# Optimization experiments

Hardware: AMD Instinct MI355X
Metric: run time of the kernel (lower is better)

Reference implementation:

```python
import jax, jax.numpy as jnp
import numpy as np

N, E, D_IN, H, L, B, D_OUT = 50000, 800000, 128, 128, 3, 512, 64
BN_EPS = 1e-5


def _leaky(v):
    return jax.nn.leaky_relu(v, 0.2)


def _bn_eval(v, g, b):
    # eval-mode BatchNorm1d with running_mean=0, running_var=1
    return g * v * (1.0 / np.sqrt(1.0 + BN_EPS)) + b


def setup_inputs() -> dict:
    key = jax.random.key(0)
    ks = jax.random.split(key, 12)
    s = 0.02  # weight init scale
    return {
        "x": jax.random.normal(ks[0], (N, D_IN), jnp.float32),
        "edge_index": jax.random.randint(ks[1], (2, E), 0, N, jnp.int64),
        "batch": jnp.sort(jax.random.randint(ks[2], (N,), 0, B, jnp.int64)),
        "node_W": jax.random.normal(ks[3], (D_IN, H), jnp.float32) * s,
        "node_b": jnp.zeros((H,), jnp.float32),
        "conv_W1": jax.random.normal(ks[4], (L, H, H), jnp.float32) * s,
        "conv_b1": jnp.zeros((L, H), jnp.float32),
        "conv_g": jnp.ones((L, H), jnp.float32),
        "conv_beta": jnp.zeros((L, H), jnp.float32),
        "conv_W2": jax.random.normal(ks[5], (L, H, H), jnp.float32) * s,
        "conv_b2": jnp.zeros((L, H), jnp.float32),
        "vn_emb": jax.random.normal(ks[6], (1, H), jnp.float32) * s,
        "vn_W1": jax.random.normal(ks[7], (L, H, H), jnp.float32) * s,
        "vn_b1": jnp.zeros((L, H), jnp.float32),
        "vn_W2": jax.random.normal(ks[8], (L, H, H), jnp.float32) * s,
        "vn_b2": jnp.zeros((L, H), jnp.float32),
        "bn_g": jnp.ones((H,), jnp.float32),
        "bn_b": jnp.zeros((H,), jnp.float32),
        "fc_W": jax.random.normal(ks[9], (D_OUT, H), jnp.float32) * s,
        "fc_b": jnp.zeros((D_OUT,), jnp.float32),
    }


def reference(x, edge_index, batch, node_W, node_b, conv_W1, conv_b1, conv_g,
              conv_beta, conv_W2, conv_b2, vn_emb, vn_W1, vn_b1, vn_W2, vn_b2,
              bn_g, bn_b, fc_W, fc_b):
    src, dst = edge_index[0], edge_index[1]
    h = x @ node_W + node_b                              # [N, H]
    vn = jnp.broadcast_to(vn_emb, (B, vn_emb.shape[1]))  # [B, H]
    counts = jax.ops.segment_sum(jnp.ones((h.shape[0],), h.dtype), batch,
                                 num_segments=B)          # [B]
    denom = jnp.maximum(counts, 1.0)[:, None]
    for l in range(L):
        h = h + vn[batch]
        # GINConv (eps=0): mlp((1+eps)*x + sum of neighbor messages)
        agg = jax.ops.segment_sum(h[src], dst, num_segments=h.shape[0])
        z = h + agg
        z = _leaky(z @ conv_W1[l] + conv_b1[l])
        z = _bn_eval(z, conv_g[l], conv_beta[l])
        h = _leaky(z @ conv_W2[l] + conv_b2[l])
        # dropout is identity in eval mode
        vn_update = jax.ops.segment_sum(h, batch, num_segments=B) / denom
        vn = vn + (_leaky(vn_update @ vn_W1[l] + vn_b1[l]) @ vn_W2[l] + vn_b2[l])
    out = jax.ops.segment_sum(h, batch, num_segments=B)   # global_add_pool
    out = _bn_eval(out, bn_g, bn_b)
    return out @ fc_W.T + fc_b                            # [B, D_OUT]
```

## Files before the change

kernel.cpp:

```cpp
#include <hip/hip_runtime.h>
#include <hip/hip_bf16.h>

#define NN 50000
#define NE 800000
#define NB 512
#define WT_S 136
#define WT_M (128 * WT_S)
#define DCAP 64

using u32 = unsigned int;
using u16 = unsigned short;
typedef __attribute__((ext_vector_type(8))) short short8;
typedef __attribute__((ext_vector_type(4))) float f32x4;

constexpr float BNS = 0.9999950000374998f;

__device__ inline u16 f2bf(float f) {
    u32 b = __builtin_bit_cast(u32, f);
    return (u16)((b + 0x7FFFu + ((b >> 16) & 1u)) >> 16);
}
__device__ inline float bf2f(u32 u) {
    return __builtin_bit_cast(float, u << 16);
}
__device__ inline u32 pk2(float a, float b) {
    return (u32)f2bf(a) | ((u32)f2bf(b) << 16);
}

__global__ void k_wprep(const float* __restrict__ nW, const float* __restrict__ cW1,
                        const float* __restrict__ cW2, u16* __restrict__ wt) {
    int idx = blockIdx.x * 256 + threadIdx.x;
    int m = idx >> 14, e = idx & 16383;
    int k = e >> 7, c = e & 127;
    const float* src = m == 0 ? nW : (m <= 3 ? cW1 + (m - 1) * 16384 : cW2 + (m - 4) * 16384);
    wt[m * WT_M + c * WT_S + k] = f2bf(src[e]);
}

__global__ void k_setup(const float* __restrict__ vn_emb, float* __restrict__ vn,
                        u16* __restrict__ vnb, const int* __restrict__ batch,
                        int* __restrict__ bstart, float* __restrict__ counts) {
    int idx = blockIdx.x * 256 + threadIdx.x;
    if (idx < NB * 128) {
        float v = vn_emb[idx & 127];
        vn[idx] = v;
        vnb[idx] = f2bf(v);
    }
    if (idx <= NB) {
        int b = idx;
        int lo = 0, hi = NN;
        while (lo < hi) { int m = (lo + hi) >> 1; if (batch[m] < b) lo = m + 1; else hi = m; }
        bstart[b] = lo;
        if (b < NB) {
            int b1 = b + 1, lo1 = 0, hi1 = NN;
            while (lo1 < hi1) { int m = (lo1 + hi1) >> 1; if (batch[m] < b1) lo1 = m + 1; else hi1 = m; }
            counts[b] = (float)(lo1 - lo);
        }
    }
}

__global__ void k_pcsr(const int* __restrict__ ei, const int* __restrict__ batch,
                       int* __restrict__ deg, u32* __restrict__ nbr) {
    int e = blockIdx.x * 256 + threadIdx.x;
    if (e >= NE) return;
    int src = ei[e];
    int dst = ei[NE + e];
    int pos = atomicAdd(&deg[dst], 1);
    if (pos < DCAP) nbr[(size_t)dst * DCAP + pos] = (u32)src | ((u32)batch[src] << 16);
}

__global__ __launch_bounds__(256) void k_gather(
    const int* __restrict__ deg, const u32* __restrict__ nbr,
    const u16* __restrict__ hb0, const u16* __restrict__ vnb,
    const int* __restrict__ batch, u16* __restrict__ ah, u16* __restrict__ alo) {
    int node = blockIdx.x * 8 + (threadIdx.x >> 5);
    int q = threadIdx.x & 31;
    if (node >= NN) return;
    const uint2* h2 = (const uint2*)hb0;
    const uint2* v2 = (const uint2*)vnb;
    const u32* nb = nbr + (size_t)node * DCAP;
    int n = min(deg[node], DCAP);
    uint2 vd = h2[(size_t)node * 32 + q];
    uint2 wd = v2[(size_t)batch[node] * 32 + q];
    float4 A = {bf2f(vd.x & 0xFFFFu) + bf2f(wd.x & 0xFFFFu),
                bf2f(vd.x >> 16) + bf2f(wd.x >> 16),
                bf2f(vd.y & 0xFFFFu) + bf2f(wd.y & 0xFFFFu),
                bf2f(vd.y >> 16) + bf2f(wd.y >> 16)};
    float4 Bc = {0.f, 0.f, 0.f, 0.f};
    int j = 0;
    for (; j + 3 < n; j += 4) {
        uint4 nn = *(const uint4*)(nb + j);
        uint2 u0 = h2[(size_t)(nn.x & 0xFFFFu) * 32 + q];
        uint2 w0 = v2[(size_t)(nn.x >> 16) * 32 + q];
        uint2 u1 = h2[(size_t)(nn.y & 0xFFFFu) * 32 + q];
        uint2 w1 = v2[(size_t)(nn.y >> 16) * 32 + q];
        uint2 u2 = h2[(size_t)(nn.z & 0xFFFFu) * 32 + q];
        uint2 w2 = v2[(size_t)(nn.z >> 16) * 32 + q];
        uint2 u3 = h2[(size_t)(nn.w & 0xFFFFu) * 32 + q];
        uint2 w3 = v2[(size_t)(nn.w >> 16) * 32 + q];
        A.x += bf2f(u0.x & 0xFFFFu) + bf2f(w0.x & 0xFFFFu);
        A.y += bf2f(u0.x >> 16) + bf2f(w0.x >> 16);
        A.z += bf2f(u0.y & 0xFFFFu) + bf2f(w0.y & 0xFFFFu);
        A.w += bf2f(u0.y >> 16) + bf2f(w0.y >> 16);
        Bc.x += bf2f(u1.x & 0xFFFFu) + bf2f(w1.x & 0xFFFFu);
        Bc.y += bf2f(u1.x >> 16) + bf2f(w1.x >> 16);
        Bc.z += bf2f(u1.y & 0xFFFFu) + bf2f(w1.y & 0xFFFFu);
        Bc.w += bf2f(u1.y >> 16) + bf2f(w1.y >> 16);
        A.x += bf2f(u2.x & 0xFFFFu) + bf2f(w2.x & 0xFFFFu);
        A.y += bf2f(u2.x >> 16) + bf2f(w2.x >> 16);
        A.z += bf2f(u2.y & 0xFFFFu) + bf2f(w2.y & 0xFFFFu);
        A.w += bf2f(u2.y >> 16) + bf2f(w2.y >> 16);
        Bc.x += bf2f(u3.x & 0xFFFFu) + bf2f(w3.x & 0xFFFFu);
        Bc.y += bf2f(u3.x >> 16) + bf2f(w3.x >> 16);
        Bc.z += bf2f(u3.y & 0xFFFFu) + bf2f(w3.y & 0xFFFFu);
        Bc.w += bf2f(u3.y >> 16) + bf2f(w3.y >> 16);
    }
    for (; j < n; ++j) {
        u32 nn = nb[j];
        uint2 u0 = h2[(size_t)(nn & 0xFFFFu) * 32 + q];
        uint2 w0 = v2[(size_t)(nn >> 16) * 32 + q];
        A.x += bf2f(u0.x & 0xFFFFu) + bf2f(w0.x & 0xFFFFu);
        A.y += bf2f(u0.x >> 16) + bf2f(w0.x >> 16);
        A.z += bf2f(u0.y & 0xFFFFu) + bf2f(w0.y & 0xFFFFu);
        A.w += bf2f(u0.y >> 16) + bf2f(w0.y >> 16);
    }
    A.x += Bc.x; A.y += Bc.y; A.z += Bc.z; A.w += Bc.w;
    u16 h0 = f2bf(A.x), h1 = f2bf(A.y), h2_ = f2bf(A.z), h3 = f2bf(A.w);
    ((uint2*)ah)[(size_t)node * 32 + q] =
        make_uint2((u32)h0 | ((u32)h1 << 16), (u32)h2_ | ((u32)h3 << 16));
    ((uint2*)alo)[(size_t)node * 32 + q] =
        make_uint2(pk2(A.x - bf2f(h0), A.y - bf2f(h1)),
                   pk2(A.z - bf2f(h2_), A.w - bf2f(h3)));
}

template <int EPI, int AMODE, bool OBF16>
__global__ __launch_bounds__(512) void k_gemm(
    const void* __restrict__ Ap, const void* __restrict__ Ap2,
    const u16* __restrict__ wt, const float* __restrict__ bias,
    const float* __restrict__ gg, const float* __restrict__ bb,
    void* __restrict__ outp, int nrows) {
    __shared__ u16 sW[WT_M];
    const int t = threadIdx.x;
    {
        const float4* src = (const float4*)wt;
        float4* dst = (float4*)sW;
        for (int i = t; i < WT_M / 8; i += 512) dst[i] = src[i];
    }
    __syncthreads();
    const int lane = t & 63;
    const int w = t >> 6;
    const int rl = lane & 15;
    const int q = lane >> 4;
    const int rbase = blockIdx.x * 256 + w * 32;

    short8 af[2][4], al[2][4];
#pragma unroll
    for (int ri = 0; ri < 2; ++ri) {
        int row = min(rbase + ri * 16 + rl, nrows - 1);
#pragma unroll
        for (int kc = 0; kc < 4; ++kc) {
            if (AMODE == 2) {
                const float* ap = (const float*)Ap + (size_t)row * 128 + kc * 32 + q * 8;
                float4 f0 = *(const float4*)ap;
                float4 f1 = *(const float4*)(ap + 4);
                float fv[8] = {f0.x, f0.y, f0.z, f0.w, f1.x, f1.y, f1.z, f1.w};
                short8 hi, lo;
#pragma unroll
                for (int i = 0; i < 8; ++i) {
                    u16 hv = f2bf(fv[i]);
                    hi[i] = (short)hv;
                    lo[i] = (short)f2bf(fv[i] - bf2f(hv));
                }
                af[ri][kc] = hi;
                al[ri][kc] = lo;
            } else {
                af[ri][kc] = *(const short8*)((const u16*)Ap + (size_t)row * 128 + kc * 32 + q * 8);
                if (AMODE == 1)
                    al[ri][kc] = *(const short8*)((const u16*)Ap2 + (size_t)row * 128 + kc * 32 + q * 8);
            }
        }
    }

#pragma unroll
    for (int ct = 0; ct < 8; ++ct) {
        f32x4 acc0 = {0.f, 0.f, 0.f, 0.f};
        f32x4 acc1 = {0.f, 0.f, 0.f, 0.f};
#pragma unroll
        for (int kc = 0; kc < 4; ++kc) {
            short8 bf = *(const short8*)&sW[(ct * 16 + rl) * WT_S + kc * 32 + q * 8];
            if (AMODE != 0) {
                acc0 = __builtin_amdgcn_mfma_f32_16x16x32_bf16(al[0][kc], bf, acc0, 0, 0, 0);
                acc1 = __builtin_amdgcn_mfma_f32_16x16x32_bf16(al[1][kc], bf, acc1, 0, 0, 0);
            }
            acc0 = __builtin_amdgcn_mfma_f32_16x16x32_bf16(af[0][kc], bf, acc0, 0, 0, 0);
            acc1 = __builtin_amdgcn_mfma_f32_16x16x32_bf16(af[1][kc], bf, acc1, 0, 0, 0);
        }
        const int col = ct * 16 + rl;
        const float bs = bias[col];
        const float g = (EPI == 2) ? gg[col] : 0.f;
        const float be = (EPI == 2) ? bb[col] : 0.f;
#pragma unroll
        for (int half = 0; half < 2; ++half) {
            const f32x4& ac = half ? acc1 : acc0;
#pragma unroll
            for (int i = 0; i < 4; ++i) {
                int r = rbase + half * 16 + q * 4 + i;
                if (r < nrows) {
                    float v = ac[i] + bs;
                    if (EPI >= 1) v = v > 0.f ? v : 0.2f * v;
                    if (EPI == 2) v = g * v * BNS + be;
                    if (OBF16) ((u16*)outp)[(size_t)r * 128 + col] = f2bf(v);
                    else ((float*)outp)[(size_t)r * 128 + col] = v;
                }
            }
        }
    }
}

__global__ __launch_bounds__(256) void k_vnup(
    const u16* __restrict__ hb0, const int* __restrict__ bstart,
    const float* __restrict__ counts, const float* __restrict__ W1,
    const float* __restrict__ b1, const float* __restrict__ W2,
    const float* __restrict__ b2, float* __restrict__ vn, u16* __restrict__ vnb) {
    __shared__ float4 red[8][32];
    __shared__ float sP[128], sT[128], sH[2][128];
    const int b = blockIdx.x;
    const int t = threadIdx.x;
    const int s = bstart[b], e = bstart[b + 1];
    const int g = t >> 5, q = t & 31;
    const uint2* h2 = (const uint2*)hb0;
    float4 a = make_float4(0.f, 0.f, 0.f, 0.f);
    for (int r = s + g; r < e; r += 8) {
        uint2 v = h2[(size_t)r * 32 + q];
        a.x += bf2f(v.x & 0xFFFFu); a.y += bf2f(v.x >> 16);
        a.z += bf2f(v.y & 0xFFFFu); a.w += bf2f(v.y >> 16);
    }
    red[g][q] = a;
    __syncthreads();
    if (g == 0) {
#pragma unroll
        for (int g2 = 1; g2 < 8; ++g2) {
            float4 v = red[g2][q];
            a.x += v.x; a.y += v.y; a.z += v.z; a.w += v.w;
        }
        float inv = 1.f / fmaxf(counts[b], 1.f);
        sP[q * 4 + 0] = a.x * inv;
        sP[q * 4 + 1] = a.y * inv;
        sP[q * 4 + 2] = a.z * inv;
        sP[q * 4 + 3] = a.w * inv;
    }
    __syncthreads();
    {
        const int c = t & 127, hf = t >> 7;
        float acc = 0.f;
        const float* Wp = W1 + (size_t)(hf * 64) * 128 + c;
#pragma unroll 8
        for (int k = 0; k < 64; ++k) acc += sP[hf * 64 + k] * Wp[(size_t)k * 128];
        sH[hf][c] = acc;
    }
    __syncthreads();
    if (t < 128) {
        float v = sH[0][t] + sH[1][t] + b1[t];
        sT[t] = v > 0.f ? v : 0.2f * v;
    }
    __syncthreads();
    {
        const int c = t & 127, hf = t >> 7;
        float acc = 0.f;
        const float* Wp = W2 + (size_t)(hf * 64) * 128 + c;
#pragma unroll 8
        for (int k = 0; k < 64; ++k) acc += sT[hf * 64 + k] * Wp[(size_t)k * 128];
        sH[hf][c] = acc;
    }
    __syncthreads();
    if (t < 128) {
        float nv = vn[(size_t)b * 128 + t] + sH[0][t] + sH[1][t] + b2[t];
        vn[(size_t)b * 128 + t] = nv;
        vnb[(size_t)b * 128 + t] = f2bf(nv);
    }
}

__global__ __launch_bounds__(256) void k_final(
    const u16* __restrict__ hb0, const int* __restrict__ bstart,
    const float* __restrict__ g, const float* __restrict__ bB,
    const float* __restrict__ fcW, const float* __restrict__ fcb,
    float* __restrict__ out) {
    __shared__ float sP[4][128];
    __shared__ float4 red[4][2][32];
    const int t = threadIdx.x;
    const int seg = t >> 6, gq = t & 63, rg = gq >> 5, q = gq & 31;
    const int b = blockIdx.x * 4 + seg;
    const int s = bstart[b], e = bstart[b + 1];
    const uint2* h2 = (const uint2*)hb0;
    float4 a = make_float4(0.f, 0.f, 0.f, 0.f);
    for (int r = s + rg; r < e; r += 2) {
        uint2 v = h2[(size_t)r * 32 + q];
        a.x += bf2f(v.x & 0xFFFFu); a.y += bf2f(v.x >> 16);
        a.z += bf2f(v.y & 0xFFFFu); a.w += bf2f(v.y >> 16);
    }
    red[seg][rg][q] = a;
    __syncthreads();
    if (rg == 0) {
        float4 v = red[seg][1][q];
        a.x += v.x; a.y += v.y; a.z += v.z; a.w += v.w;
        float av[4] = {a.x, a.y, a.z, a.w};
#pragma unroll
        for (int i = 0; i < 4; ++i) {
            int c = q * 4 + i;
            sP[seg][c] = g[c] * av[i] * BNS + bB[c];
        }
    }
    __syncthreads();
    const int o = t & 63;
    float acc = fcb[o];
    const float* wrow = fcW + o * 128;
    const float* prow = sP[seg];
    for (int k = 0; k < 128; ++k) acc += prow[k] * wrow[k];
    out[(size_t)b * 64 + o] = acc;
}

extern "C" void kernel_launch(void* const* d_in, const int* in_sizes, int n_in,
                              void* d_out, int out_size, void* d_ws, size_t ws_size,
                              hipStream_t stream) {
    const float* x       = (const float*)d_in[0];
    const int*   ei      = (const int*)d_in[1];
    const int*   batch   = (const int*)d_in[2];
    const float* node_W  = (const float*)d_in[3];
    const float* node_b  = (const float*)d_in[4];
    const float* conv_W1 = (const float*)d_in[5];
    const float* conv_b1 = (const float*)d_in[6];
    const float* conv_g  = (const float*)d_in[7];
    const float* conv_bt = (const float*)d_in[8];
    const float* conv_W2 = (const float*)d_in[9];
    const float* conv_b2 = (const float*)d_in[10];
    const float* vn_emb  = (const float*)d_in[11];
    const float* vn_W1   = (const float*)d_in[12];
    const float* vn_b1   = (const float*)d_in[13];
    const float* vn_W2   = (const float*)d_in[14];
    const float* vn_b2   = (const float*)d_in[15];
    const float* bn_g    = (const float*)d_in[16];
    const float* bn_b    = (const float*)d_in[17];
    const float* fc_W    = (const float*)d_in[18];
    const float* fc_b    = (const float*)d_in[19];
    float* out = (float*)d_out;

    char* ws = (char*)d_ws;
    u16* hb0   = (u16*)ws;
    u16* aggh  = hb0 + (size_t)NN * 128;
    u16* agglo = aggh + (size_t)NN * 128;
    u16* wt    = agglo + (size_t)NN * 128;
    u32* nbr   = (u32*)(wt + 7 * WT_M);
    float* vn  = (float*)(nbr + (size_t)NN * DCAP);
    u16* vnb   = (u16*)(vn + NB * 128);
    float* counts = (float*)(vnb + NB * 128);
    int* bstart = (int*)(counts + NB);
    int* deg    = bstart + NB + 1;

    hipMemsetAsync(deg, 0, NN * sizeof(int), stream);
    k_wprep<<<448, 256, 0, stream>>>(node_W, conv_W1, conv_W2, wt);
    k_pcsr<<<(NE + 255) / 256, 256, 0, stream>>>(ei, batch, deg, nbr);
    k_setup<<<(NB * 128 + 255) / 256, 256, 0, stream>>>(vn_emb, vn, vnb, batch, bstart, counts);

    const int GG = (NN + 255) / 256;

    k_gemm<0, 2, true><<<GG, 512, 0, stream>>>(
        x, nullptr, wt, node_b, nullptr, nullptr, hb0, NN);

    for (int l = 0; l < 3; ++l) {
        k_gather<<<(NN + 7) / 8, 256, 0, stream>>>(deg, nbr, hb0, vnb, batch, aggh, agglo);
        k_gemm<2, 1, true><<<GG, 512, 0, stream>>>(
            aggh, agglo, wt + (size_t)(1 + l) * WT_M, conv_b1 + l * 128,
            conv_g + l * 128, conv_bt + l * 128, aggh, NN);
        k_gemm<1, 0, true><<<GG, 512, 0, stream>>>(
            aggh, nullptr, wt + (size_t)(4 + l) * WT_M, conv_b2 + l * 128,
            nullptr, nullptr, hb0, NN);
        if (l < 2)
            k_vnup<<<NB, 256, 0, stream>>>(hb0, bstart, counts, vn_W1 + l * 16384,
                                           vn_b1 + l * 128, vn_W2 + l * 16384,
                                           vn_b2 + l * 128, vn, vnb);
    }

    k_final<<<NB / 4, 256, 0, stream>>>(hb0, bstart, bn_g, bn_b, fc_W, fc_b, out);
}
```

Baseline: 348.0 us.

## Fuse GIN MLP's two GEMMs into one kernel and merge setup kernels

Merges the CSR build, weight prep and setup into a single launch, dispatching work by block index. Fuses each layer's two 128x128 GEMMs into one k_conv kernel. The intermediate z is staged as bf16 in shared memory instead of round-tripping through global memory. The second GEMM reads its weights straight from global/L2 rather than from LDS. Blocks shrink to 128 rows and 256 threads, which changes occupancy and how often weights are reloaded.

```diff
diff --git a/kernel.cpp b/kernel.cpp
--- a/kernel.cpp
+++ b/kernel.cpp
@@ -7,6 +7,8 @@
 #define WT_S 136
 #define WT_M (128 * WT_S)
 #define DCAP 64
+#define PCSRB ((NE + 255) / 256)
+#define PREPB 704
 
 using u32 = unsigned int;
 using u16 = unsigned short;
@@ -26,19 +28,32 @@
     return (u32)f2bf(a) | ((u32)f2bf(b) << 16);
 }
 
-__global__ void k_wprep(const float* __restrict__ nW, const float* __restrict__ cW1,
-                        const float* __restrict__ cW2, u16* __restrict__ wt) {
-    int idx = blockIdx.x * 256 + threadIdx.x;
-    int m = idx >> 14, e = idx & 16383;
-    int k = e >> 7, c = e & 127;
-    const float* src = m == 0 ? nW : (m <= 3 ? cW1 + (m - 1) * 16384 : cW2 + (m - 4) * 16384);
-    wt[m * WT_M + c * WT_S + k] = f2bf(src[e]);
-}
-
-__global__ void k_setup(const float* __restrict__ vn_emb, float* __restrict__ vn,
-                        u16* __restrict__ vnb, const int* __restrict__ batch,
-                        int* __restrict__ bstart, float* __restrict__ counts) {
-    int idx = blockIdx.x * 256 + threadIdx.x;
+__global__ void k_build(const int* __restrict__ ei, const int* __restrict__ batch,
+                        int* __restrict__ deg, u32* __restrict__ nbr,
+                        const float* __restrict__ nW, const float* __restrict__ cW1,
+                        const float* __restrict__ cW2, u16* __restrict__ wt,
+                        const float* __restrict__ vn_emb, float* __restrict__ vn,
+                        u16* __restrict__ vnb, int* __restrict__ bstart,
+                        float* __restrict__ counts) {
+    if (blockIdx.x < PCSRB) {
+        int e = blockIdx.x * 256 + threadIdx.x;
+        if (e >= NE) return;
+        int src = ei[e];
+        int dst = ei[NE + e];
+        int pos = atomicAdd(&deg[dst], 1);
+        if (pos < DCAP) nbr[(size_t)dst * DCAP + pos] = (u32)src | ((u32)batch[src] << 16);
+        return;
+    }
+    int bb = blockIdx.x - PCSRB;
+    if (bb < 448) {
+        int idx = bb * 256 + threadIdx.x;
+        int m = idx >> 14, e = idx & 16383;
+        int k = e >> 7, c = e & 127;
+        const float* src = m == 0 ? nW : (m <= 3 ? cW1 + (m - 1) * 16384 : cW2 + (m - 4) * 16384);
+        wt[m * WT_M + c * WT_S + k] = f2bf(src[e]);
+        return;
+    }
+    int idx = (bb - 448) * 256 + threadIdx.x;
     if (idx < NB * 128) {
         float v = vn_emb[idx & 127];
         vn[idx] = v;
@@ -55,16 +70,6 @@
             counts[b] = (float)(lo1 - lo);
         }
     }
-}
-
-__global__ void k_pcsr(const int* __restrict__ ei, const int* __restrict__ batch,
-                       int* __restrict__ deg, u32* __restrict__ nbr) {
-    int e = blockIdx.x * 256 + threadIdx.x;
-    if (e >= NE) return;
-    int src = ei[e];
-    int dst = ei[NE + e];
-    int pos = atomicAdd(&deg[dst], 1);
-    if (pos < DCAP) nbr[(size_t)dst * DCAP + pos] = (u32)src | ((u32)batch[src] << 16);
 }
 
 __global__ __launch_bounds__(256) void k_gather(
@@ -131,12 +136,9 @@
                    pk2(A.z - bf2f(h2_), A.w - bf2f(h3)));
 }
 
-template <int EPI, int AMODE, bool OBF16>
-__global__ __launch_bounds__(512) void k_gemm(
-    const void* __restrict__ Ap, const void* __restrict__ Ap2,
-    const u16* __restrict__ wt, const float* __restrict__ bias,
-    const float* __restrict__ gg, const float* __restrict__ bb,
-    void* __restrict__ outp, int nrows) {
+__global__ __launch_bounds__(512) void k_gemm0(
+    const float* __restrict__ Ap, const u16* __restrict__ wt,
+    const float* __restrict__ bias, u16* __restrict__ outp) {
     __shared__ u16 sW[WT_M];
     const int t = threadIdx.x;
     {
@@ -154,28 +156,22 @@
     short8 af[2][4], al[2][4];
 #pragma unroll
     for (int ri = 0; ri < 2; ++ri) {
-        int row = min(rbase + ri * 16 + rl, nrows - 1);
+        int row = min(rbase + ri * 16 + rl, NN - 1);
 #pragma unroll
         for (int kc = 0; kc < 4; ++kc) {
-            if (AMODE == 2) {
-                const float* ap = (const float*)Ap + (size_t)row * 128 + kc * 32 + q * 8;
-                float4 f0 = *(const float4*)ap;
-                float4 f1 = *(const float4*)(ap + 4);
-                float fv[8] = {f0.x, f0.y, f0.z, f0.w, f1.x, f1.y, f1.z, f1.w};
-                short8 hi, lo;
-#pragma unroll
-                for (int i = 0; i < 8; ++i) {
-                    u16 hv = f2bf(fv[i]);
-                    hi[i] = (short)hv;
-                    lo[i] = (short)f2bf(fv[i] - bf2f(hv));
-                }
-                af[ri][kc] = hi;
-                al[ri][kc] = lo;
-            } else {
-                af[ri][kc] = *(const short8*)((const u16*)Ap + (size_t)row * 128 + kc * 32 + q * 8);
-                if (AMODE == 1)
-                    al[ri][kc] = *(const short8*)((const u16*)Ap2 + (size_t)row * 128 + kc * 32 + q * 8);
+            const float* ap = Ap + (size_t)row * 128 + kc * 32 + q * 8;
+            float4 f0 = *(const float4*)ap;
+            float4 f1 = *(const float4*)(ap + 4);
+            float fv[8] = {f0.x, f0.y, f0.z, f0.w, f1.x, f1.y, f1.z, f1.w};
+            short8 hi, lo;
+#pragma unroll
+            for (int i = 0; i < 8; ++i) {
+                u16 hv = f2bf(fv[i]);
+                hi[i] = (short)hv;
+                lo[i] = (short)f2bf(fv[i] - bf2f(hv));
             }
+            af[ri][kc] = hi;
+            al[ri][kc] = lo;
         }
     }
 
@@ -186,29 +182,126 @@
 #pragma unroll
         for (int kc = 0; kc < 4; ++kc) {
             short8 bf = *(const short8*)&sW[(ct * 16 + rl) * WT_S + kc * 32 + q * 8];
-            if (AMODE != 0) {
-                acc0 = __builtin_amdgcn_mfma_f32_16x16x32_bf16(al[0][kc], bf, acc0, 0, 0, 0);
-                acc1 = __builtin_amdgcn_mfma_f32_16x16x32_bf16(al[1][kc], bf, acc1, 0, 0, 0);
-            }
+            acc0 = __builtin_amdgcn_mfma_f32_16x16x32_bf16(al[0][kc], bf, acc0, 0, 0, 0);
+            acc1 = __builtin_amdgcn_mfma_f32_16x16x32_bf16(al[1][kc], bf, acc1, 0, 0, 0);
             acc0 = __builtin_amdgcn_mfma_f32_16x16x32_bf16(af[0][kc], bf, acc0, 0, 0, 0);
             acc1 = __builtin_amdgcn_mfma_f32_16x16x32_bf16(af[1][kc], bf, acc1, 0, 0, 0);
         }
         const int col = ct * 16 + rl;
         const float bs = bias[col];
-        const float g = (EPI == 2) ? gg[col] : 0.f;
-        const float be = (EPI == 2) ? bb[col] : 0.f;
 #pragma unroll
         for (int half = 0; half < 2; ++half) {
             const f32x4& ac = half ? acc1 : acc0;
 #pragma unroll
             for (int i = 0; i < 4; ++i) {
                 int r = rbase + half * 16 + q * 4 + i;
-                if (r < nrows) {
+                if (r < NN) outp[(size_t)r * 128 + col] = f2bf(ac[i] + bs);
+            }
+        }
+    }
+}
+
+__global__ __launch_bounds__(256) void k_conv(
+    const u16* __restrict__ aggh, const u16* __restrict__ agglo,
+    const u16* __restrict__ wt1, const float* __restrict__ bias1,
+    const float* __restrict__ gg, const float* __restrict__ bb,
+    const u16* __restrict__ wt2, const float* __restrict__ bias2,
+    u16* __restrict__ hb0) {
+    __shared__ u16 sZ[WT_M];
+    const int t = threadIdx.x;
+    const int lane = t & 63;
+    const int w = t >> 6;
+    const int rl = lane & 15;
+    const int q = lane >> 4;
+    const int lbase = w * 32;
+    const int rbase = blockIdx.x * 128 + lbase;
+
+    short8 af[2][4], al[2][4];
+#pragma unroll
+    for (int ri = 0; ri < 2; ++ri) {
+        int row = min(rbase + ri * 16 + rl, NN - 1);
+#pragma unroll
+        for (int kc = 0; kc < 4; ++kc) {
+            af[ri][kc] = *(const short8*)(aggh + (size_t)row * 128 + kc * 32 + q * 8);
+            al[ri][kc] = *(const short8*)(agglo + (size_t)row * 128 + kc * 32 + q * 8);
+        }
+    }
+    {
+        const float4* src = (const float4*)wt1;
+        float4* dst = (float4*)sZ;
+        for (int i = t; i < WT_M / 8; i += 256) dst[i] = src[i];
+    }
+    __syncthreads();
+
+    float zs[8][8];
+#pragma unroll
+    for (int ct = 0; ct < 8; ++ct) {
+        f32x4 acc0 = {0.f, 0.f, 0.f, 0.f};
+        f32x4 acc1 = {0.f, 0.f, 0.f, 0.f};
+#pragma unroll
+        for (int kc = 0; kc < 4; ++kc) {
+            short8 bf = *(const short8*)&sZ[(ct * 16 + rl) * WT_S + kc * 32 + q * 8];
+            acc0 = __builtin_amdgcn_mfma_f32_16x16x32_bf16(al[0][kc], bf, acc0, 0, 0, 0);
+            acc1 = __builtin_amdgcn_mfma_f32_16x16x32_bf16(al[1][kc], bf, acc1, 0, 0, 0);
+            acc0 = __builtin_amdgcn_mfma_f32_16x16x32_bf16(af[0][kc], bf, acc0, 0, 0, 0);
+            acc1 = __builtin_amdgcn_mfma_f32_16x16x32_bf16(af[1][kc], bf, acc1, 0, 0, 0);
+        }
+        const int col = ct * 16 + rl;
+        const float bs = bias1[col];
+        const float g = gg[col];
+        const float be = bb[col];
+#pragma unroll
+        for (int i = 0; i < 4; ++i) {
+            float v0 = acc0[i] + bs;
+            v0 = v0 > 0.f ? v0 : 0.2f * v0;
+            zs[ct][i] = g * v0 * BNS + be;
+            float v1 = acc1[i] + bs;
+            v1 = v1 > 0.f ? v1 : 0.2f * v1;
+            zs[ct][4 + i] = g * v1 * BNS + be;
+        }
+    }
+    __syncthreads();
+
+#pragma unroll
+    for (int ct = 0; ct < 8; ++ct) {
+        const int col = ct * 16 + rl;
+#pragma unroll
+        for (int i = 0; i < 4; ++i) {
+            sZ[(lbase + q * 4 + i) * WT_S + col] = f2bf(zs[ct][i]);
+            sZ[(lbase + 16 + q * 4 + i) * WT_S + col] = f2bf(zs[ct][4 + i]);
+        }
+    }
+    __syncthreads();
+
+    short8 zf[2][4];
+#pragma unroll
+    for (int ri = 0; ri < 2; ++ri)
+#pragma unroll
+        for (int kc = 0; kc < 4; ++kc)
+            zf[ri][kc] = *(const short8*)&sZ[(lbase + ri * 16 + rl) * WT_S + kc * 32 + q * 8];
+
+#pragma unroll
+    for (int ct = 0; ct < 8; ++ct) {
+        f32x4 acc0 = {0.f, 0.f, 0.f, 0.f};
+        f32x4 acc1 = {0.f, 0.f, 0.f, 0.f};
+#pragma unroll
+        for (int kc = 0; kc < 4; ++kc) {
+            short8 bf = *(const short8*)(wt2 + (size_t)(ct * 16 + rl) * WT_S + kc * 32 + q * 8);
+            acc0 = __builtin_amdgcn_mfma_f32_16x16x32_bf16(zf[0][kc], bf, acc0, 0, 0, 0);
+            acc1 = __builtin_amdgcn_mfma_f32_16x16x32_bf16(zf[1][kc], bf, acc1, 0, 0, 0);
+        }
+        const int col = ct * 16 + rl;
+        const float bs = bias2[col];
+#pragma unroll
+        for (int half = 0; half < 2; ++half) {
+            const f32x4& ac = half ? acc1 : acc0;
+#pragma unroll
+            for (int i = 0; i < 4; ++i) {
+                int r = rbase + half * 16 + q * 4 + i;
+                if (r < NN) {
                     float v = ac[i] + bs;
-                    if (EPI >= 1) v = v > 0.f ? v : 0.2f * v;
-                    if (EPI == 2) v = g * v * BNS + be;
-                    if (OBF16) ((u16*)outp)[(size_t)r * 128 + col] = f2bf(v);
-                    else ((float*)outp)[(size_t)r * 128 + col] = v;
+                    v = v > 0.f ? v : 0.2f * v;
+                    hb0[(size_t)r * 128 + col] = f2bf(v);
                 }
             }
         }
@@ -355,23 +448,17 @@
     int* deg    = bstart + NB + 1;
 
     hipMemsetAsync(deg, 0, NN * sizeof(int), stream);
-    k_wprep<<<448, 256, 0, stream>>>(node_W, conv_W1, conv_W2, wt);
-    k_pcsr<<<(NE + 255) / 256, 256, 0, stream>>>(ei, batch, deg, nbr);
-    k_setup<<<(NB * 128 + 255) / 256, 256, 0, stream>>>(vn_emb, vn, vnb, batch, bstart, counts);
-
-    const int GG = (NN + 255) / 256;
-
-    k_gemm<0, 2, true><<<GG, 512, 0, stream>>>(
-        x, nullptr, wt, node_b, nullptr, nullptr, hb0, NN);
+    k_build<<<PCSRB + PREPB, 256, 0, stream>>>(ei, batch, deg, nbr, node_W, conv_W1,
+                                               conv_W2, wt, vn_emb, vn, vnb, bstart, counts);
+
+    k_gemm0<<<(NN + 255) / 256, 512, 0, stream>>>(x, wt, node_b, hb0);
 
     for (int l = 0; l < 3; ++l) {
         k_gather<<<(NN + 7) / 8, 256, 0, stream>>>(deg, nbr, hb0, vnb, batch, aggh, agglo);
-        k_gemm<2, 1, true><<<GG, 512, 0, stream>>>(
+        k_conv<<<(NN + 127) / 128, 256, 0, stream>>>(
             aggh, agglo, wt + (size_t)(1 + l) * WT_M, conv_b1 + l * 128,
-            conv_g + l * 128, conv_bt + l * 128, aggh, NN);
-        k_gemm<1, 0, true><<<GG, 512, 0, stream>>>(
-            aggh, nullptr, wt + (size_t)(4 + l) * WT_M, conv_b2 + l * 128,
-            nullptr, nullptr, hb0, NN);
+            conv_g + l * 128, conv_bt + l * 128,
+            wt + (size_t)(4 + l) * WT_M, conv_b2 + l * 128, hb0);
         if (l < 2)
             k_vnup<<<NB, 256, 0, stream>>>(hb0, bstart, counts, vn_W1 + l * 16384,
                                            vn_b1 + l * 128, vn_W2 + l * 16384,
```

Measured after the change: 311.1 us. 1.12x faster.
